# Optimization experiments

Measured on AMD Instinct MI355X. Metric: run time of the kernel, lower is better.

The kernel has to match this reference:

```python
import jax, jax.numpy as jnp
import numpy as np


def setup_inputs() -> dict:
    key = jax.random.key(0)
    ks = jax.random.split(key, 12)
    Tq, Tk, B, H = 1024, 1024, 8, 1024
    inp = {
        "inputs_q": jax.random.normal(ks[0], (Tq, B, H), jnp.float32),
        "inputs_kv": jax.random.normal(ks[1], (Tk, B, H), jnp.float32),
        "w_q": jax.random.normal(ks[2], (H, H), jnp.float32) * 0.02,
        "b_q": jnp.zeros((H,), jnp.float32),
        "w_kv": jax.random.normal(ks[3], (2 * H, H), jnp.float32) * 0.02,
        "b_kv": jnp.zeros((2 * H,), jnp.float32),
        "w_o": jax.random.normal(ks[4], (H, H), jnp.float32) * 0.02,
        "b_o": jnp.zeros((H,), jnp.float32),
        # BatchEnsemble rank-1 factors, initialized near 1
        "r_q": 1.0 + 0.05 * jax.random.normal(ks[5], (B, H), jnp.float32),
        "s_q": 1.0 + 0.05 * jax.random.normal(ks[6], (B, H), jnp.float32),
        "r_kv": 1.0 + 0.05 * jax.random.normal(ks[7], (B, H), jnp.float32),
        "s_kv": 1.0 + 0.05 * jax.random.normal(ks[8], (B, 2 * H), jnp.float32),
        "heads": 16,
    }
    return inp


def be_linear(x, w, b, r, s):
    # x: [T,B,Hin], w: [Hout,Hin], r: [B,Hin], s: [B,Hout]
    return jnp.einsum('tbh,oh->tbo', x * r, w) * s + b


def reference(inputs_q, inputs_kv, w_q, b_q, w_kv, b_kv, w_o, b_o,
              r_q, s_q, r_kv, s_kv, heads):
    Tq, B, H = inputs_q.shape
    Tk = inputs_kv.shape[0]
    hd = H // heads
    scale = hd ** -0.5

    q = be_linear(inputs_q, w_q, b_q, r_q, s_q)          # [Tq,B,H]
    kv = be_linear(inputs_kv, w_kv, b_kv, r_kv, s_kv)    # [Tk,B,2H]

    queries = q.reshape(Tq, B * heads, hd)
    kv = kv.reshape(Tk, B * heads, 2, hd)                # layout: head x {k,v} x hd
    keys = kv[:, :, 0, :]
    values = kv[:, :, 1, :]

    scores = jnp.einsum('qnd,knd->nqk', queries, keys) * scale  # [B*heads,Tq,Tk]
    probs = jax.nn.softmax(scores.astype(jnp.float32), axis=-1).astype(scores.dtype)
    # dropout_prob = 0 / eval: dropout is identity
    ctx = jnp.einsum('nqk,knd->qnd', probs, values).reshape(Tq, B, H)
    out = jnp.einsum('tbh,oh->tbo', ctx, w_o) + b_o      # [Tq,B,H]
    return out
```

## Files before the change

kernel.cpp:

```cpp
#include <hip/hip_runtime.h>
#include <stdint.h>

typedef unsigned short u16;
typedef __bf16 bf16x8 __attribute__((ext_vector_type(8)));
typedef float f32x4 __attribute__((ext_vector_type(4)));

typedef __attribute__((address_space(3))) void lds_void;
typedef const __attribute__((address_space(1))) void gbl_void;
#define GLD_LDS16(g, l) __builtin_amdgcn_global_load_lds((gbl_void*)(g), (lds_void*)(l), 16, 0, 0)

__device__ __forceinline__ u16 f2bf(float f) {
  unsigned u = __float_as_uint(f);
  u += 0x7fffu + ((u >> 16) & 1u);
  return (u16)(u >> 16);
}

__device__ __forceinline__ unsigned pk2bf(float a, float b) {
  unsigned au = __float_as_uint(a) + 0x8000u;
  unsigned bu = __float_as_uint(b) + 0x8000u;
  return __builtin_amdgcn_perm(bu, au, 0x07060302u);
}

__global__ void k_convert_all(const float* __restrict__ inq, const float* __restrict__ r_q,
                              const float* __restrict__ inkv, const float* __restrict__ r_kv,
                              const float* __restrict__ w_q, const float* __restrict__ w_kv,
                              const float* __restrict__ w_o,
                              u16* __restrict__ Xq, u16* __restrict__ Xkv,
                              u16* __restrict__ Wq, u16* __restrict__ Wkv,
                              u16* __restrict__ Wo) {
  int blk = blockIdx.x;
  const float* src; const float* r = nullptr; u16* dst; int base;
  if (blk < 8192)       { src = inq;  r = r_q;  dst = Xq;  base = 0; }
  else if (blk < 16384) { src = inkv; r = r_kv; dst = Xkv; base = 8192; }
  else if (blk < 17408) { src = w_q;  dst = Wq;  base = 16384; }
  else if (blk < 19456) { src = w_kv; dst = Wkv; base = 17408; }
  else                  { src = w_o;  dst = Wo;  base = 19456; }
  int i4 = ((blk - base) * 256 + threadIdx.x) * 4;
  float4 xv = *(const float4*)(src + i4);
  if (r) {
    int rb = ((i4 >> 10) & 7) * 1024 + (i4 & 1023);
    float4 rv = *(const float4*)(r + rb);
    xv.x *= rv.x; xv.y *= rv.y; xv.z *= rv.z; xv.w *= rv.w;
  }
  unsigned long long pk = (unsigned long long)pk2bf(xv.x, xv.y)
      | ((unsigned long long)pk2bf(xv.z, xv.w) << 32);
  *(unsigned long long*)(dst + i4) = pk;
}

template <int MODE>
__global__ void k_gemm_bt(const u16* __restrict__ A, const u16* __restrict__ B,
                          void* __restrict__ Cout, const float* __restrict__ s,
                          const float* __restrict__ bias, int M, int N, int K,
                          float postscale) {
  __shared__ __align__(16) u16 As[128 * 32];
  __shared__ __align__(16) u16 Bs[128 * 32];
  const int tid = threadIdx.x;
  const int w = tid >> 6, lane = tid & 63;
  const int quad = lane >> 4, l16 = lane & 15;
  const int n0 = blockIdx.x * 128, m0 = blockIdx.y * 128;
  const int wm = (w & 1) * 64, wn = (w >> 1) * 64;

  f32x4 acc[4][4] = {};

  int srow[2], scol[2];
#pragma unroll
  for (int i = 0; i < 2; ++i) {
    int p = (w * 2 + i) * 64 + lane;
    int row = p >> 2;
    int cb = (p & 3) ^ ((row >> 1) & 3);
    srow[i] = row; scol[i] = cb * 8;
  }
  int offA[4], offB[4];
#pragma unroll
  for (int t = 0; t < 4; ++t) {
    int ra = wm + t * 16 + l16;
    offA[t] = ra * 32 + ((quad ^ ((ra >> 1) & 3)) * 8);
    int rb = wn + t * 16 + l16;
    offB[t] = rb * 32 + ((quad ^ ((rb >> 1) & 3)) * 8);
  }

  for (int k0 = 0; k0 < K; k0 += 32) {
#pragma unroll
    for (int i = 0; i < 2; ++i) {
      GLD_LDS16(A + (size_t)(m0 + srow[i]) * K + k0 + scol[i], As + (w * 2 + i) * 512);
      GLD_LDS16(B + (size_t)(n0 + srow[i]) * K + k0 + scol[i], Bs + (w * 2 + i) * 512);
    }
    __syncthreads();
    bf16x8 af[4], bfr[4];
#pragma unroll
    for (int mt = 0; mt < 4; ++mt) af[mt] = *(const bf16x8*)(As + offA[mt]);
#pragma unroll
    for (int nt = 0; nt < 4; ++nt) bfr[nt] = *(const bf16x8*)(Bs + offB[nt]);
#pragma unroll
    for (int mt = 0; mt < 4; ++mt)
#pragma unroll
      for (int nt = 0; nt < 4; ++nt)
        acc[mt][nt] = __builtin_amdgcn_mfma_f32_16x16x32_bf16(af[mt], bfr[nt], acc[mt][nt], 0, 0, 0);
    __syncthreads();
  }

#pragma unroll
  for (int mt = 0; mt < 4; ++mt)
#pragma unroll
    for (int nt = 0; nt < 4; ++nt) {
      int n = n0 + wn + nt * 16 + l16;
#pragma unroll
      for (int rg = 0; rg < 4; ++rg) {
        int m = m0 + wm + mt * 16 + quad * 4 + rg;
        float v = acc[mt][nt][rg];
        if (MODE == 0) {
          v = (v * s[(m & 7) * N + n] + bias[n]) * postscale;
          ((u16*)Cout)[(size_t)m * N + n] = f2bf(v);
        } else {
          ((float*)Cout)[(size_t)m * N + n] = v + bias[n];
        }
      }
    }
}

__global__ void k_transpose_v(const u16* __restrict__ kv, u16* __restrict__ vt) {
  __shared__ __align__(16) u16 tile[64][72];
  const int tid = threadIdx.x;
  const int n = blockIdx.x >> 4;
  const int t0 = (blockIdx.x & 15) << 6;
#pragma unroll
  for (int it = 0; it < 2; ++it) {
    int r = it * 32 + (tid >> 3);
    int c = (tid & 7) << 3;
    *(uint4*)&tile[r][c] = *(const uint4*)(kv + ((size_t)(t0 + r) * 128 + n) * 128 + 64 + c);
  }
  __syncthreads();
#pragma unroll
  for (int it = 0; it < 2; ++it) {
    int d = it * 32 + (tid >> 3);
    int tc = (tid & 7) << 3;
    u16 v[8];
#pragma unroll
    for (int j = 0; j < 8; ++j) v[j] = tile[tc + j][d];
    uint4 o;
    o.x = (unsigned)v[0] | ((unsigned)v[1] << 16);
    o.y = (unsigned)v[2] | ((unsigned)v[3] << 16);
    o.z = (unsigned)v[4] | ((unsigned)v[5] << 16);
    o.w = (unsigned)v[6] | ((unsigned)v[7] << 16);
    *(uint4*)(vt + ((size_t)n * 64 + d) * 1024 + t0 + tc) = o;
  }
}

__global__ __launch_bounds__(512, 4) void k_attn(const u16* __restrict__ qb,
                                                 const u16* __restrict__ kvb,
                                                 const u16* __restrict__ vtb,
                                                 u16* __restrict__ ctx) {
  __shared__ __align__(16) u16 Ks[2][64 * 64];
  __shared__ __align__(16) u16 Vts[2][64 * 64];
  __shared__ __align__(16) u16 Ps[8][16 * 72];

  const int tid = threadIdx.x;
  const int w = tid >> 6, lane = tid & 63;
  const int quad = lane >> 4, l16 = lane & 15;
  const int n = blockIdx.x & 127;
  const int q0 = (blockIdx.x >> 7) << 7;
  const int tq = q0 + w * 16 + l16;

  bf16x8 bq[2];
#pragma unroll
  for (int ks = 0; ks < 2; ++ks)
    bq[ks] = *(const bf16x8*)(qb + ((size_t)tq * 128 + n) * 64 + ks * 32 + quad * 8);

  const int wv = w & 3;
  int sr[2], scb[2];
#pragma unroll
  for (int i = 0; i < 2; ++i) {
    int p = (wv * 2 + i) * 64 + lane;
    sr[i] = p >> 3;
    scb[i] = ((p & 7) ^ (sr[i] & 7)) * 8;
  }

  const bool isK = (w < 4);
  const u16* gbase[2];
  u16* lbase[2];
#pragma unroll
  for (int i = 0; i < 2; ++i) {
    if (isK) {
      gbase[i] = kvb + ((size_t)sr[i] * 128 + n) * 128 + scb[i];
      lbase[i] = &Ks[0][(wv * 2 + i) * 512];
    } else {
      gbase[i] = vtb + ((size_t)n * 64 + sr[i]) * 1024 + scb[i];
      lbase[i] = &Vts[0][(wv * 2 + i) * 512];
    }
  }
  const size_t gstep = isK ? 16384 : 1;
  const int lstep = 64 * 64;

  float l_i = 0.f;
  f32x4 accO[4] = {};
  u16* myP = Ps[w];
  const int pbase = l16 * 72;

#pragma unroll
  for (int i = 0; i < 2; ++i) GLD_LDS16(gbase[i], lbase[i]);

#pragma unroll 1
  for (int tk0 = 0; tk0 < 1024; tk0 += 64) {
    const int cur = (tk0 >> 6) & 1;
    __syncthreads();

    if (tk0 < 960) {
      size_t goff = (size_t)(tk0 + 64) * gstep;
#pragma unroll
      for (int i = 0; i < 2; ++i)
        GLD_LDS16(gbase[i] + goff, lbase[i] + (cur ^ 1) * lstep);
    }

    const u16* Kc = Ks[cur];
    const u16* Vc = Vts[cur];

    f32x4 accS[4] = {};
#pragma unroll
    for (int mt = 0; mt < 4; ++mt) {
      int r = mt * 16 + l16;
#pragma unroll
      for (int ks = 0; ks < 2; ++ks) {
        bf16x8 ak = *(const bf16x8*)(Kc + r * 64 + (((ks * 4 + quad) ^ (r & 7)) << 3));
        accS[mt] = __builtin_amdgcn_mfma_f32_16x16x32_bf16(ak, bq[ks], accS[mt], 0, 0, 0);
      }
    }

    float pv[16];
    float s0 = 0.f, s1 = 0.f;
#pragma unroll
    for (int mt = 0; mt < 4; ++mt)
#pragma unroll
      for (int rg = 0; rg < 4; ++rg) {
        float p = __builtin_amdgcn_exp2f(accS[mt][rg]);
        pv[mt * 4 + rg] = p;
        if (rg & 1) s1 += p; else s0 += p;
      }
    float ssum = s0 + s1;
    ssum += __shfl_xor(ssum, 16);
    ssum += __shfl_xor(ssum, 32);
    l_i += ssum;

#pragma unroll
    for (int mt = 0; mt < 4; ++mt) {
      unsigned long long pk = (unsigned long long)pk2bf(pv[mt * 4 + 0], pv[mt * 4 + 1])
          | ((unsigned long long)pk2bf(pv[mt * 4 + 2], pv[mt * 4 + 3]) << 32);
      *(unsigned long long*)(myP + pbase + mt * 16 + quad * 4) = pk;
    }
#pragma unroll
    for (int dt = 0; dt < 4; ++dt) {
      int r = dt * 16 + l16;
#pragma unroll
      for (int ks = 0; ks < 2; ++ks) {
        bf16x8 av = *(const bf16x8*)(Vc + r * 64 + (((ks * 4 + quad) ^ (r & 7)) << 3));
        bf16x8 bp = *(const bf16x8*)(myP + pbase + ks * 32 + quad * 8);
        accO[dt] = __builtin_amdgcn_mfma_f32_16x16x32_bf16(av, bp, accO[dt], 0, 0, 0);
      }
    }
  }

  float inv = 1.f / l_i;
#pragma unroll
  for (int dt = 0; dt < 4; ++dt) {
    unsigned long long pk = (unsigned long long)pk2bf(accO[dt][0] * inv, accO[dt][1] * inv)
        | ((unsigned long long)pk2bf(accO[dt][2] * inv, accO[dt][3] * inv) << 32);
    *(unsigned long long*)(ctx + ((size_t)tq * 128 + n) * 64 + dt * 16 + quad * 4) = pk;
  }
}

extern "C" void kernel_launch(void* const* d_in, const int* in_sizes, int n_in,
                              void* d_out, int out_size, void* d_ws, size_t ws_size,
                              hipStream_t stream) {
  const float* inq  = (const float*)d_in[0];
  const float* inkv = (const float*)d_in[1];
  const float* w_q  = (const float*)d_in[2];
  const float* b_q  = (const float*)d_in[3];
  const float* w_kv = (const float*)d_in[4];
  const float* b_kv = (const float*)d_in[5];
  const float* w_o  = (const float*)d_in[6];
  const float* b_o  = (const float*)d_in[7];
  const float* r_q  = (const float*)d_in[8];
  const float* s_q  = (const float*)d_in[9];
  const float* r_kv = (const float*)d_in[10];
  const float* s_kv = (const float*)d_in[11];

  const size_t MEG = 1024 * 1024;
  u16* ws    = (u16*)d_ws;
  u16* Xq    = ws;
  u16* Xkv   = ws + 8 * MEG;
  u16* Wq    = ws + 16 * MEG;
  u16* Wkv   = ws + 17 * MEG;
  u16* Wo    = ws + 19 * MEG;
  u16* qbuf  = ws + 20 * MEG;
  u16* kvbuf = ws + 28 * MEG;
  u16* vt    = Xkv;
  u16* ctx   = Xq;

  k_convert_all<<<20480, 256, 0, stream>>>(inq, r_q, inkv, r_kv, w_q, w_kv, w_o,
                                           Xq, Xkv, Wq, Wkv, Wo);

  const float QSCALE = 0.125f * 1.44269504088896340736f;
  k_gemm_bt<0><<<dim3(8, 64), 256, 0, stream>>>(Xq, Wq, qbuf, s_q, b_q, 8192, 1024, 1024, QSCALE);
  k_gemm_bt<0><<<dim3(16, 64), 256, 0, stream>>>(Xkv, Wkv, kvbuf, s_kv, b_kv, 8192, 2048, 1024, 1.0f);
  k_transpose_v<<<2048, 256, 0, stream>>>(kvbuf, vt);
  k_attn<<<1024, 512, 0, stream>>>(qbuf, kvbuf, vt, ctx);
  k_gemm_bt<1><<<dim3(8, 64), 256, 0, stream>>>(ctx, Wo, d_out, nullptr, b_o, 8192, 1024, 1024, 1.0f);
}
```

Baseline: 314.8 us.

## Double-buffer GEMM LDS, merge Q/KV GEMMs, and give attention waves two query tiles

The GEMM tile loop now double-buffers its LDS tiles, so the next K-slice load is issued before computing on the current one, and one barrier per iteration is removed. The Q and KV projection GEMMs are merged into a single launch with a combined grid. The attention kernel moves from 8 waves per block handling 16 queries each to 4 waves handling 32 queries each, so every K/V fragment read from LDS feeds two MFMAs. The trade-off is higher register pressure and fewer waves per block in attention.

```diff
diff --git a/kernel.cpp b/kernel.cpp
--- a/kernel.cpp
+++ b/kernel.cpp
@@ -48,16 +48,14 @@
 }
 
 template <int MODE>
-__global__ void k_gemm_bt(const u16* __restrict__ A, const u16* __restrict__ B,
-                          void* __restrict__ Cout, const float* __restrict__ s,
-                          const float* __restrict__ bias, int M, int N, int K,
-                          float postscale) {
-  __shared__ __align__(16) u16 As[128 * 32];
-  __shared__ __align__(16) u16 Bs[128 * 32];
-  const int tid = threadIdx.x;
+__device__ __forceinline__ void gemm_tile(const u16* __restrict__ A, const u16* __restrict__ B,
+                                          void* __restrict__ Cout, const float* __restrict__ s,
+                                          const float* __restrict__ bias, int N, int K,
+                                          float postscale, int bx, int by,
+                                          u16* As, u16* Bs, int tid) {
   const int w = tid >> 6, lane = tid & 63;
   const int quad = lane >> 4, l16 = lane & 15;
-  const int n0 = blockIdx.x * 128, m0 = blockIdx.y * 128;
+  const int n0 = bx * 128, m0 = by * 128;
   const int wm = (w & 1) * 64, wn = (w >> 1) * 64;
 
   f32x4 acc[4][4] = {};
@@ -79,24 +77,36 @@
     offB[t] = rb * 32 + ((quad ^ ((rb >> 1) & 3)) * 8);
   }
 
+#pragma unroll
+  for (int i = 0; i < 2; ++i) {
+    GLD_LDS16(A + (size_t)(m0 + srow[i]) * K + scol[i], As + (w * 2 + i) * 512);
+    GLD_LDS16(B + (size_t)(n0 + srow[i]) * K + scol[i], Bs + (w * 2 + i) * 512);
+  }
+
   for (int k0 = 0; k0 < K; k0 += 32) {
-#pragma unroll
-    for (int i = 0; i < 2; ++i) {
-      GLD_LDS16(A + (size_t)(m0 + srow[i]) * K + k0 + scol[i], As + (w * 2 + i) * 512);
-      GLD_LDS16(B + (size_t)(n0 + srow[i]) * K + k0 + scol[i], Bs + (w * 2 + i) * 512);
-    }
+    const int cur = (k0 >> 5) & 1;
     __syncthreads();
+    if (k0 + 32 < K) {
+#pragma unroll
+      for (int i = 0; i < 2; ++i) {
+        GLD_LDS16(A + (size_t)(m0 + srow[i]) * K + (k0 + 32) + scol[i],
+                  As + (cur ^ 1) * 4096 + (w * 2 + i) * 512);
+        GLD_LDS16(B + (size_t)(n0 + srow[i]) * K + (k0 + 32) + scol[i],
+                  Bs + (cur ^ 1) * 4096 + (w * 2 + i) * 512);
+      }
+    }
+    const u16* Ac = As + cur * 4096;
+    const u16* Bc = Bs + cur * 4096;
     bf16x8 af[4], bfr[4];
 #pragma unroll
-    for (int mt = 0; mt < 4; ++mt) af[mt] = *(const bf16x8*)(As + offA[mt]);
-#pragma unroll
-    for (int nt = 0; nt < 4; ++nt) bfr[nt] = *(const bf16x8*)(Bs + offB[nt]);
+    for (int mt = 0; mt < 4; ++mt) af[mt] = *(const bf16x8*)(Ac + offA[mt]);
+#pragma unroll
+    for (int nt = 0; nt < 4; ++nt) bfr[nt] = *(const bf16x8*)(Bc + offB[nt]);
 #pragma unroll
     for (int mt = 0; mt < 4; ++mt)
 #pragma unroll
       for (int nt = 0; nt < 4; ++nt)
         acc[mt][nt] = __builtin_amdgcn_mfma_f32_16x16x32_bf16(af[mt], bfr[nt], acc[mt][nt], 0, 0, 0);
-    __syncthreads();
   }
 
 #pragma unroll
@@ -118,6 +128,27 @@
     }
 }
 
+__global__ void k_gemm_qkv(const u16* __restrict__ Xq, const u16* __restrict__ Wq,
+                           u16* __restrict__ qout, const float* __restrict__ s_q,
+                           const float* __restrict__ b_q, float qscale,
+                           const u16* __restrict__ Xkv, const u16* __restrict__ Wkv,
+                           u16* __restrict__ kvout, const float* __restrict__ s_kv,
+                           const float* __restrict__ b_kv) {
+  __shared__ __align__(16) u16 As[2 * 4096];
+  __shared__ __align__(16) u16 Bs[2 * 4096];
+  if (blockIdx.x < 8)
+    gemm_tile<0>(Xq, Wq, qout, s_q, b_q, 1024, 1024, qscale, blockIdx.x, blockIdx.y, As, Bs, threadIdx.x);
+  else
+    gemm_tile<0>(Xkv, Wkv, kvout, s_kv, b_kv, 2048, 1024, 1.0f, blockIdx.x - 8, blockIdx.y, As, Bs, threadIdx.x);
+}
+
+__global__ void k_gemm_o(const u16* __restrict__ A, const u16* __restrict__ B,
+                         float* __restrict__ Cout, const float* __restrict__ bias) {
+  __shared__ __align__(16) u16 As[2 * 4096];
+  __shared__ __align__(16) u16 Bs[2 * 4096];
+  gemm_tile<1>(A, B, Cout, nullptr, bias, 1024, 1024, 1.0f, blockIdx.x, blockIdx.y, As, Bs, threadIdx.x);
+}
+
 __global__ void k_transpose_v(const u16* __restrict__ kv, u16* __restrict__ vt) {
   __shared__ __align__(16) u16 tile[64][72];
   const int tid = threadIdx.x;
@@ -146,124 +177,134 @@
   }
 }
 
-__global__ __launch_bounds__(512, 4) void k_attn(const u16* __restrict__ qb,
+__global__ __launch_bounds__(256, 3) void k_attn(const u16* __restrict__ qb,
                                                  const u16* __restrict__ kvb,
                                                  const u16* __restrict__ vtb,
                                                  u16* __restrict__ ctx) {
-  __shared__ __align__(16) u16 Ks[2][64 * 64];
-  __shared__ __align__(16) u16 Vts[2][64 * 64];
-  __shared__ __align__(16) u16 Ps[8][16 * 72];
+  __shared__ __align__(16) u16 Ks[2][4096];
+  __shared__ __align__(16) u16 Vts[2][4096];
+  __shared__ __align__(16) u16 Ps[4][32 * 72];
 
   const int tid = threadIdx.x;
   const int w = tid >> 6, lane = tid & 63;
   const int quad = lane >> 4, l16 = lane & 15;
   const int n = blockIdx.x & 127;
   const int q0 = (blockIdx.x >> 7) << 7;
-  const int tq = q0 + w * 16 + l16;
-
-  bf16x8 bq[2];
-#pragma unroll
-  for (int ks = 0; ks < 2; ++ks)
-    bq[ks] = *(const bf16x8*)(qb + ((size_t)tq * 128 + n) * 64 + ks * 32 + quad * 8);
-
-  const int wv = w & 3;
-  int sr[2], scb[2];
-#pragma unroll
-  for (int i = 0; i < 2; ++i) {
-    int p = (wv * 2 + i) * 64 + lane;
-    sr[i] = p >> 3;
-    scb[i] = ((p & 7) ^ (sr[i] & 7)) * 8;
-  }
-
-  const bool isK = (w < 4);
-  const u16* gbase[2];
-  u16* lbase[2];
-#pragma unroll
-  for (int i = 0; i < 2; ++i) {
+  const int qw = q0 + w * 32;
+
+  bf16x8 bq[2][2];
+#pragma unroll
+  for (int g = 0; g < 2; ++g)
+#pragma unroll
+    for (int ks = 0; ks < 2; ++ks)
+      bq[g][ks] = *(const bf16x8*)(qb + ((size_t)(qw + g * 16 + l16) * 128 + n) * 64 + ks * 32 + quad * 8);
+
+  const bool isK = (w < 2);
+  const int wv = w & 1;
+  const u16* gbase[4];
+  u16* lbase[4];
+#pragma unroll
+  for (int i = 0; i < 4; ++i) {
+    int p = (wv * 4 + i) * 64 + lane;
+    int r = p >> 3;
+    int scb = ((p & 7) ^ (r & 7)) * 8;
     if (isK) {
-      gbase[i] = kvb + ((size_t)sr[i] * 128 + n) * 128 + scb[i];
-      lbase[i] = &Ks[0][(wv * 2 + i) * 512];
+      gbase[i] = kvb + ((size_t)r * 128 + n) * 128 + scb;
+      lbase[i] = &Ks[0][(wv * 4 + i) * 512];
     } else {
-      gbase[i] = vtb + ((size_t)n * 64 + sr[i]) * 1024 + scb[i];
-      lbase[i] = &Vts[0][(wv * 2 + i) * 512];
+      gbase[i] = vtb + ((size_t)n * 64 + r) * 1024 + scb;
+      lbase[i] = &Vts[0][(wv * 4 + i) * 512];
     }
   }
   const size_t gstep = isK ? 16384 : 1;
-  const int lstep = 64 * 64;
-
-  float l_i = 0.f;
-  f32x4 accO[4] = {};
+  const int lstep = 4096;
+
+  float l_i[2] = {0.f, 0.f};
+  f32x4 accO[2][4] = {};
   u16* myP = Ps[w];
-  const int pbase = l16 * 72;
-
-#pragma unroll
-  for (int i = 0; i < 2; ++i) GLD_LDS16(gbase[i], lbase[i]);
+
+#pragma unroll
+  for (int i = 0; i < 4; ++i) GLD_LDS16(gbase[i], lbase[i]);
 
 #pragma unroll 1
   for (int tk0 = 0; tk0 < 1024; tk0 += 64) {
     const int cur = (tk0 >> 6) & 1;
     __syncthreads();
-
     if (tk0 < 960) {
       size_t goff = (size_t)(tk0 + 64) * gstep;
 #pragma unroll
-      for (int i = 0; i < 2; ++i)
+      for (int i = 0; i < 4; ++i)
         GLD_LDS16(gbase[i] + goff, lbase[i] + (cur ^ 1) * lstep);
     }
-
     const u16* Kc = Ks[cur];
     const u16* Vc = Vts[cur];
 
-    f32x4 accS[4] = {};
+    f32x4 accS[2][4] = {};
 #pragma unroll
     for (int mt = 0; mt < 4; ++mt) {
       int r = mt * 16 + l16;
 #pragma unroll
       for (int ks = 0; ks < 2; ++ks) {
         bf16x8 ak = *(const bf16x8*)(Kc + r * 64 + (((ks * 4 + quad) ^ (r & 7)) << 3));
-        accS[mt] = __builtin_amdgcn_mfma_f32_16x16x32_bf16(ak, bq[ks], accS[mt], 0, 0, 0);
-      }
-    }
-
-    float pv[16];
-    float s0 = 0.f, s1 = 0.f;
-#pragma unroll
-    for (int mt = 0; mt < 4; ++mt)
-#pragma unroll
-      for (int rg = 0; rg < 4; ++rg) {
-        float p = __builtin_amdgcn_exp2f(accS[mt][rg]);
-        pv[mt * 4 + rg] = p;
-        if (rg & 1) s1 += p; else s0 += p;
-      }
-    float ssum = s0 + s1;
-    ssum += __shfl_xor(ssum, 16);
-    ssum += __shfl_xor(ssum, 32);
-    l_i += ssum;
-
-#pragma unroll
-    for (int mt = 0; mt < 4; ++mt) {
-      unsigned long long pk = (unsigned long long)pk2bf(pv[mt * 4 + 0], pv[mt * 4 + 1])
-          | ((unsigned long long)pk2bf(pv[mt * 4 + 2], pv[mt * 4 + 3]) << 32);
-      *(unsigned long long*)(myP + pbase + mt * 16 + quad * 4) = pk;
-    }
+#pragma unroll
+        for (int g = 0; g < 2; ++g)
+          accS[g][mt] = __builtin_amdgcn_mfma_f32_16x16x32_bf16(ak, bq[g][ks], accS[g][mt], 0, 0, 0);
+      }
+    }
+
+#pragma unroll
+    for (int g = 0; g < 2; ++g) {
+      float pv[16];
+      float ss = 0.f;
+#pragma unroll
+      for (int mt = 0; mt < 4; ++mt)
+#pragma unroll
+        for (int rg = 0; rg < 4; ++rg) {
+          float p = __builtin_amdgcn_exp2f(accS[g][mt][rg]);
+          pv[mt * 4 + rg] = p;
+          ss += p;
+        }
+      ss += __shfl_xor(ss, 16);
+      ss += __shfl_xor(ss, 32);
+      l_i[g] += ss;
+      const int prow = (g * 16 + l16) * 72;
+#pragma unroll
+      for (int mt = 0; mt < 4; ++mt) {
+        unsigned long long pk = (unsigned long long)pk2bf(pv[mt * 4 + 0], pv[mt * 4 + 1])
+            | ((unsigned long long)pk2bf(pv[mt * 4 + 2], pv[mt * 4 + 3]) << 32);
+        *(unsigned long long*)(myP + prow + mt * 16 + quad * 4) = pk;
+      }
+    }
+
+    bf16x8 bp[2][2];
+#pragma unroll
+    for (int g = 0; g < 2; ++g)
+#pragma unroll
+      for (int ks = 0; ks < 2; ++ks)
+        bp[g][ks] = *(const bf16x8*)(myP + (g * 16 + l16) * 72 + ks * 32 + quad * 8);
 #pragma unroll
     for (int dt = 0; dt < 4; ++dt) {
       int r = dt * 16 + l16;
 #pragma unroll
       for (int ks = 0; ks < 2; ++ks) {
         bf16x8 av = *(const bf16x8*)(Vc + r * 64 + (((ks * 4 + quad) ^ (r & 7)) << 3));
-        bf16x8 bp = *(const bf16x8*)(myP + pbase + ks * 32 + quad * 8);
-        accO[dt] = __builtin_amdgcn_mfma_f32_16x16x32_bf16(av, bp, accO[dt], 0, 0, 0);
-      }
-    }
-  }
-
-  float inv = 1.f / l_i;
-#pragma unroll
-  for (int dt = 0; dt < 4; ++dt) {
-    unsigned long long pk = (unsigned long long)pk2bf(accO[dt][0] * inv, accO[dt][1] * inv)
-        | ((unsigned long long)pk2bf(accO[dt][2] * inv, accO[dt][3] * inv) << 32);
-    *(unsigned long long*)(ctx + ((size_t)tq * 128 + n) * 64 + dt * 16 + quad * 4) = pk;
+#pragma unroll
+        for (int g = 0; g < 2; ++g)
+          accO[g][dt] = __builtin_amdgcn_mfma_f32_16x16x32_bf16(av, bp[g][ks], accO[g][dt], 0, 0, 0);
+      }
+    }
+  }
+
+#pragma unroll
+  for (int g = 0; g < 2; ++g) {
+    float inv = 1.f / l_i[g];
+    const size_t obase = ((size_t)(qw + g * 16 + l16) * 128 + n) * 64;
+#pragma unroll
+    for (int dt = 0; dt < 4; ++dt) {
+      unsigned long long pk = (unsigned long long)pk2bf(accO[g][dt][0] * inv, accO[g][dt][1] * inv)
+          | ((unsigned long long)pk2bf(accO[g][dt][2] * inv, accO[g][dt][3] * inv) << 32);
+      *(unsigned long long*)(ctx + obase + dt * 16 + quad * 4) = pk;
+    }
   }
 }
 
@@ -299,9 +340,9 @@
                                            Xq, Xkv, Wq, Wkv, Wo);
 
   const float QSCALE = 0.125f * 1.44269504088896340736f;
-  k_gemm_bt<0><<<dim3(8, 64), 256, 0, stream>>>(Xq, Wq, qbuf, s_q, b_q, 8192, 1024, 1024, QSCALE);
-  k_gemm_bt<0><<<dim3(16, 64), 256, 0, stream>>>(Xkv, Wkv, kvbuf, s_kv, b_kv, 8192, 2048, 1024, 1.0f);
+  k_gemm_qkv<<<dim3(24, 64), 256, 0, stream>>>(Xq, Wq, qbuf, s_q, b_q, QSCALE,
+                                               Xkv, Wkv, kvbuf, s_kv, b_kv);
   k_transpose_v<<<2048, 256, 0, stream>>>(kvbuf, vt);
-  k_attn<<<1024, 512, 0, stream>>>(qbuf, kvbuf, vt, ctx);
-  k_gemm_bt<1><<<dim3(8, 64), 256, 0, stream>>>(ctx, Wo, d_out, nullptr, b_o, 8192, 1024, 1024, 1.0f);
-}
+  k_attn<<<1024, 256, 0, stream>>>(qbuf, kvbuf, vt, ctx);
+  k_gemm_o<<<dim3(8, 64), 256, 0, stream>>>(ctx, Wo, (float*)d_out, b_o);
+}
```

After: 300.0 us. 4.7% less time.
